# Kernel tuning notes

Measured on AMD Instinct MI355X. Metric: run time of the kernel, lower is better.

The kernel has to match this reference:

```python
import jax, jax.numpy as jnp
import numpy as np

NUM_HEADS = 8
HEAD_DIM = 64
GROUPS = 32
EPS = 1e-5


def setup_inputs() -> dict:
    key = jax.random.key(0)
    ks = jax.random.split(key, 7)
    B, C, H, W = 8, 512, 32, 32
    x = jax.random.normal(ks[0], (B, C, H, W), dtype=jnp.float32)
    gn_w = jnp.ones((C,), dtype=jnp.float32)
    gn_b = jnp.zeros((C,), dtype=jnp.float32)
    # 1x1 convs stored as [out, in] matrices
    qkv_w = jax.random.normal(ks[1], (3 * C, C), dtype=jnp.float32) * (1.0 / np.sqrt(C))
    qkv_b = jnp.zeros((3 * C,), dtype=jnp.float32)
    proj_w = jax.random.normal(ks[2], (C, C), dtype=jnp.float32) * (1.0 / np.sqrt(C))
    proj_b = jnp.zeros((C,), dtype=jnp.float32)
    return {"x": x, "gn_w": gn_w, "gn_b": gn_b, "qkv_w": qkv_w,
            "qkv_b": qkv_b, "proj_w": proj_w, "proj_b": proj_b}


def _group_norm(x, w, b):
    B, C, H, W = x.shape
    xg = x.reshape(B, GROUPS, C // GROUPS, H, W)
    mu = xg.mean(axis=(2, 3, 4), keepdims=True)
    var = xg.var(axis=(2, 3, 4), keepdims=True)
    xn = ((xg - mu) * jax.lax.rsqrt(var + EPS)).reshape(B, C, H, W)
    return xn * w[None, :, None, None] + b[None, :, None, None]


def reference(x, gn_w, gn_b, qkv_w, qkv_b, proj_w, proj_b):
    B, C, H, W = x.shape
    N = H * W
    h = _group_norm(x, gn_w, gn_b)
    # 1x1 conv == per-pixel matmul: [B, 3C, N]
    hf = h.reshape(B, C, N)
    qkv = jnp.einsum('oc,bcn->bon', qkv_w, hf) + qkv_b[None, :, None]
    qkv = qkv.reshape(B, 3, NUM_HEADS, HEAD_DIM, N)
    q, k, v = qkv[:, 0], qkv[:, 1], qkv[:, 2]  # each [B, h, d, N]
    attn = jnp.einsum('bhdi,bhdj->bhij', q, k) * (HEAD_DIM ** -0.5)
    attn = jax.nn.softmax(attn, axis=-1)
    out = jnp.einsum('bhij,bhdj->bhdi', attn, v)  # [B, h, d, N]
    out = out.reshape(B, C, N)
    out = jnp.einsum('oc,bcn->bon', proj_w, out) + proj_b[None, :, None]
    return x + out.reshape(B, C, H, W)
```

## Files before the change

### kernel.cpp

```cpp
#include <hip/hip_runtime.h>
#include <hip/hip_bf16.h>

#define BF16 __hip_bfloat16

typedef __attribute__((ext_vector_type(8))) short bf16x8;
typedef __attribute__((ext_vector_type(4))) float f32x4;
typedef __attribute__((ext_vector_type(4))) unsigned short ushort4v;
typedef __attribute__((ext_vector_type(4))) float float4v;

__device__ __forceinline__ unsigned short f2bf(float f) {
  BF16 h = __float2bfloat16(f);
  union { BF16 h; unsigned short u; } cv;
  cv.h = h;
  return cv.u;
}

__device__ __forceinline__ void gload_lds16(const BF16* g, BF16* s) {
  __builtin_amdgcn_global_load_lds(
      (const __attribute__((address_space(1))) void*)g,
      (__attribute__((address_space(3))) void*)s, 16, 0, 0);
}

__global__ __launch_bounds__(256) void cast_w_kernel(const float* __restrict__ qw,
                                                     const float* __restrict__ pw,
                                                     BF16* __restrict__ wq,
                                                     BF16* __restrict__ wp) {
  int i = blockIdx.x * 256 + threadIdx.x;
  if (i < 1536 * 512) wq[i] = __float2bfloat16(qw[i]);
  if (i < 512 * 512)  wp[i] = __float2bfloat16(pw[i]);
}

__global__ __launch_bounds__(256) void gn_kernel(const float* __restrict__ x,
                                                 const float* __restrict__ gw,
                                                 const float* __restrict__ gb,
                                                 BF16* __restrict__ h_t) {
  const int blk = blockIdx.x;
  const int bb = blk >> 5, g = blk & 31;
  const float* xg = x + (size_t)(bb * 512 + g * 16) * 1024;

  float s = 0.f, ss = 0.f;
  const float4v* x4 = (const float4v*)xg;
  for (int i = threadIdx.x; i < 4096; i += 256) {
    float4v v = x4[i];
    s  += v[0] + v[1] + v[2] + v[3];
    ss += v[0] * v[0] + v[1] * v[1] + v[2] * v[2] + v[3] * v[3];
  }
  for (int off = 32; off > 0; off >>= 1) {
    s  += __shfl_down(s, off, 64);
    ss += __shfl_down(ss, off, 64);
  }
  __shared__ float sred[8];
  const int wv = threadIdx.x >> 6;
  if ((threadIdx.x & 63) == 0) { sred[wv] = s; sred[4 + wv] = ss; }
  __syncthreads();
  const float S  = sred[0] + sred[1] + sred[2] + sred[3];
  const float SS = sred[4] + sred[5] + sred[6] + sred[7];
  const float mean = S * (1.f / 16384.f);
  const float var  = SS * (1.f / 16384.f) - mean * mean;
  const float rstd = rsqrtf(var + 1e-5f);

  const int ci = threadIdx.x & 15, nb = threadIdx.x >> 4;
  const int c  = g * 16 + ci;
  const float aw = gw[c] * rstd;
  const float ab = gb[c] - mean * aw;
  const float* xrow = xg + (size_t)ci * 1024;
  BF16* hb = h_t + (size_t)bb * 1024 * 512 + c;
  #pragma unroll 4
  for (int i = 0; i < 64; ++i) {
    int n = nb + i * 16;
    hb[(size_t)n * 512] = __float2bfloat16(aw * xrow[n] + ab);
  }
}

#define GEMM_PROLOGUE()                                                        \
  const int tid = threadIdx.x, l = tid & 63, wv = tid >> 6;                    \
  const int wm = wv >> 1, wn = wv & 1;                                         \
  const int lc = l & 15, lh = l >> 4;                                          \
  __shared__ __align__(16) BF16 Al[128 * 64];                                  \
  __shared__ __align__(16) BF16 Bl[128 * 64];                                  \
  f32x4 acc[4][4] = {};                                                        \
  int srow[4], scg[4];                                                         \
  _Pragma("unroll")                                                            \
  for (int t = 0; t < 4; ++t) {                                                \
    int cidx = t * 256 + wv * 64 + l;            \
    srow[t] = cidx >> 3;                                                       \
    scg[t]  = (cidx & 7) ^ (srow[t] & 7);    \
  }                                                                            \
  for (int kt = 0; kt < 8; ++kt) {                                             \
    const int k0 = kt * 64;                                                    \
    __syncthreads();                                                           \
    _Pragma("unroll")                                                          \
    for (int t = 0; t < 4; ++t) {                                              \
      gload_lds16(&A[(size_t)srow[t] * 512 + k0 + scg[t] * 8],                 \
                  &Al[(t * 256 + wv * 64) * 8]);                               \
      gload_lds16(&B[(size_t)srow[t] * 512 + k0 + scg[t] * 8],                 \
                  &Bl[(t * 256 + wv * 64) * 8]);                               \
    }                                                                          \
    __syncthreads();                                                           \
    _Pragma("unroll")                                                          \
    for (int ks = 0; ks < 2; ++ks) {                                           \
      bf16x8 af[4], bfr[4];                                                    \
      _Pragma("unroll")                                                        \
      for (int i = 0; i < 4; ++i) {                                            \
        int rA = wm * 64 + i * 16 + lc;                                        \
        int cA = (ks * 4 + lh) ^ (rA & 7);                                     \
        af[i] = *(const bf16x8*)&Al[(rA * 8 + cA) * 8];                        \
        int rB = wn * 64 + i * 16 + lc;                                        \
        int cB = (ks * 4 + lh) ^ (rB & 7);                                     \
        bfr[i] = *(const bf16x8*)&Bl[(rB * 8 + cB) * 8];                       \
      }                                                                        \
      _Pragma("unroll")                                                        \
      for (int i = 0; i < 4; ++i)                                              \
        _Pragma("unroll")                                                      \
        for (int j = 0; j < 4; ++j)                                            \
          acc[i][j] = __builtin_amdgcn_mfma_f32_16x16x32_bf16(af[i], bfr[j],   \
                                                              acc[i][j], 0, 0, 0); \
    }                                                                          \
  }

__global__ __launch_bounds__(256) void qkv_gemm_kernel(const BF16* __restrict__ Wq,
                                                       const BF16* __restrict__ Ht,
                                                       const float* __restrict__ bias,
                                                       BF16* __restrict__ q_t,
                                                       BF16* __restrict__ k_t,
                                                       BF16* __restrict__ v_nat) {
  const int nt = blockIdx.x, mt = blockIdx.y, b = blockIdx.z;
  const int m0 = mt * 128, n0 = nt * 128;
  const BF16* A = Wq + (size_t)m0 * 512;
  const BF16* B = Ht + (size_t)b * 1024 * 512 + (size_t)n0 * 512;
  GEMM_PROLOGUE()

  const int r0 = lh * 4;
  #pragma unroll
  for (int mi = 0; mi < 4; ++mi) {
    const int o = m0 + wm * 64 + mi * 16 + r0;
    #pragma unroll
    for (int ni = 0; ni < 4; ++ni) {
      const int pix = n0 + wn * 64 + ni * 16 + lc;
      f32x4 a = acc[mi][ni];
      if (mt < 8) {
        const float scale = (mt < 4) ? 0.125f : 1.0f;
        const int hh = (o >> 6) & 7;
        const int d = o & 63;
        BF16* dst = (mt < 4 ? q_t : k_t) +
                    ((size_t)(b * 8 + hh) * 1024 + pix) * 64 + d;
        ushort4v pk;
        #pragma unroll
        for (int r = 0; r < 4; ++r) pk[r] = f2bf((a[r] + bias[o + r]) * scale);
        *(ushort4v*)dst = pk;
      } else {
        #pragma unroll
        for (int r = 0; r < 4; ++r) {
          const int vr = o + r - 1024;
          v_nat[((size_t)(b * 512 + vr)) * 1024 + pix] =
              __float2bfloat16(a[r] + bias[o + r]);
        }
      }
    }
  }
}

__global__ __launch_bounds__(256) void proj_gemm_kernel(const BF16* __restrict__ Wp,
                                                        const BF16* __restrict__ At,
                                                        const float* __restrict__ bias,
                                                        const float* __restrict__ x,
                                                        float* __restrict__ out) {
  const int nt = blockIdx.x, mt = blockIdx.y, b = blockIdx.z;
  const int m0 = mt * 128, n0 = nt * 128;
  const BF16* A = Wp + (size_t)m0 * 512;
  const BF16* B = At + (size_t)b * 1024 * 512 + (size_t)n0 * 512;
  GEMM_PROLOGUE()

  const int r0 = lh * 4;
  #pragma unroll
  for (int mi = 0; mi < 4; ++mi) {
    #pragma unroll
    for (int ni = 0; ni < 4; ++ni) {
      const int n = n0 + wn * 64 + ni * 16 + lc;
      f32x4 a = acc[mi][ni];
      #pragma unroll
      for (int r = 0; r < 4; ++r) {
        const int c = m0 + wm * 64 + mi * 16 + r0 + r;
        const size_t idx = ((size_t)(b * 512 + c)) * 1024 + n;
        out[idx] = x[idx] + bias[c] + a[r];
      }
    }
  }
}

__global__ __launch_bounds__(256) void attn_kernel(const BF16* __restrict__ q_t,
                                                   const BF16* __restrict__ k_t,
                                                   const BF16* __restrict__ v_nat,
                                                   BF16* __restrict__ attout) {
  const int bh = blockIdx.y;
  const int b = bh >> 3, hh = bh & 7;
  const int i0 = blockIdx.x * 64;
  const int tid = threadIdx.x, l = tid & 63, wv = tid >> 6;
  const int lc = l & 15, lh = l >> 4;

  __shared__ __align__(16) BF16 Kl[2][64 * 64];
  __shared__ __align__(16) BF16 Vl[2][64 * 64];
  __shared__ __align__(16) BF16 Pl[4][16][72];

  bf16x8 aq0, aq1;
  {
    const BF16* qp = q_t + ((size_t)bh * 1024 + i0 + wv * 16 + lc) * 64;
    aq0 = *(const bf16x8*)&qp[lh * 8];
    aq1 = *(const bf16x8*)&qp[32 + lh * 8];
  }

  f32x4 O[4] = {};
  float mr = -1e30f, lr = 0.f;

  const BF16* kbase = k_t + (size_t)bh * 1024 * 64;
  const BF16* vbase = v_nat + (size_t)bh * 64 * 1024;

  int srow[2], scg[2];
  #pragma unroll
  for (int it = 0; it < 2; ++it) {
    int cidx = it * 256 + wv * 64 + l;
    srow[it] = cidx >> 3;
    scg[it]  = (cidx & 7) ^ (srow[it] & 7);
  }

  #pragma unroll
  for (int it = 0; it < 2; ++it) {
    gload_lds16(&kbase[(size_t)srow[it] * 64 + scg[it] * 8],
                &Kl[0][(it * 256 + wv * 64) * 8]);
    gload_lds16(&vbase[(size_t)srow[it] * 1024 + scg[it] * 8],
                &Vl[0][(it * 256 + wv * 64) * 8]);
  }

  for (int jt = 0; jt < 16; ++jt) {
    const int cur = jt & 1;
    __syncthreads();
    if (jt < 15) {
      const int j1 = (jt + 1) * 64, nxt = cur ^ 1;
      #pragma unroll
      for (int it = 0; it < 2; ++it) {
        gload_lds16(&kbase[(size_t)(j1 + srow[it]) * 64 + scg[it] * 8],
                    &Kl[nxt][(it * 256 + wv * 64) * 8]);
        gload_lds16(&vbase[(size_t)srow[it] * 1024 + j1 + scg[it] * 8],
                    &Vl[nxt][(it * 256 + wv * 64) * 8]);
      }
    }

    f32x4 Sv[4];
    __builtin_amdgcn_s_setprio(1);
    #pragma unroll
    for (int jf = 0; jf < 4; ++jf) {
      const int jl = jf * 16 + lc;
      int c0 = lh ^ (jl & 7);
      bf16x8 ak = *(const bf16x8*)&Kl[cur][(jl * 8 + c0) * 8];
      f32x4 s0 = {};
      s0 = __builtin_amdgcn_mfma_f32_16x16x32_bf16(ak, aq0, s0, 0, 0, 0);
      int c1 = (4 + lh) ^ (jl & 7);
      ak = *(const bf16x8*)&Kl[cur][(jl * 8 + c1) * 8];
      Sv[jf] = __builtin_amdgcn_mfma_f32_16x16x32_bf16(ak, aq1, s0, 0, 0, 0);
    }
    __builtin_amdgcn_s_setprio(0);

    float tmax = Sv[0][0];
    #pragma unroll
    for (int jf = 0; jf < 4; ++jf)
      #pragma unroll
      for (int r = 0; r < 4; ++r) tmax = fmaxf(tmax, Sv[jf][r]);
    tmax = fmaxf(tmax, __shfl_xor(tmax, 16, 64));
    tmax = fmaxf(tmax, __shfl_xor(tmax, 32, 64));
    const float mnew = fmaxf(mr, tmax);
    const float sc = __expf(mr - mnew);
    mr = mnew;
    float rs = 0.f;
    float p[4][4];
    #pragma unroll
    for (int jf = 0; jf < 4; ++jf)
      #pragma unroll
      for (int r = 0; r < 4; ++r) {
        p[jf][r] = __expf(Sv[jf][r] - mnew);
        rs += p[jf][r];
      }
    rs += __shfl_xor(rs, 16, 64);
    rs += __shfl_xor(rs, 32, 64);
    lr = lr * sc + rs;
    #pragma unroll
    for (int nf = 0; nf < 4; ++nf)
      #pragma unroll
      for (int r = 0; r < 4; ++r) O[nf][r] *= sc;

    #pragma unroll
    for (int jf = 0; jf < 4; ++jf) {
      ushort4v pk;
      #pragma unroll
      for (int r = 0; r < 4; ++r) pk[r] = f2bf(p[jf][r]);
      *(ushort4v*)&Pl[wv][lc][jf * 16 + 4 * lh] = pk;
    }
    const bf16x8 bp0 = *(const bf16x8*)&Pl[wv][lc][lh * 8];
    const bf16x8 bp1 = *(const bf16x8*)&Pl[wv][lc][32 + lh * 8];

    __builtin_amdgcn_s_setprio(1);
    #pragma unroll
    for (int nf = 0; nf < 4; ++nf) {
      const int dl = nf * 16 + lc;
      int c0 = lh ^ (dl & 7);
      bf16x8 av = *(const bf16x8*)&Vl[cur][(dl * 8 + c0) * 8];
      O[nf] = __builtin_amdgcn_mfma_f32_16x16x32_bf16(av, bp0, O[nf], 0, 0, 0);
      int c1 = (4 + lh) ^ (dl & 7);
      av = *(const bf16x8*)&Vl[cur][(dl * 8 + c1) * 8];
      O[nf] = __builtin_amdgcn_mfma_f32_16x16x32_bf16(av, bp1, O[nf], 0, 0, 0);
    }
    __builtin_amdgcn_s_setprio(0);
  }

  const float inv = 1.0f / lr;
  BF16* dst = attout + ((size_t)b * 1024 + i0 + wv * 16 + lc) * 512 + hh * 64;
  #pragma unroll
  for (int nf = 0; nf < 4; ++nf) {
    ushort4v pk;
    #pragma unroll
    for (int r = 0; r < 4; ++r) pk[r] = f2bf(O[nf][r] * inv);
    *(ushort4v*)&dst[nf * 16 + 4 * lh] = pk;
  }
}

extern "C" void kernel_launch(void* const* d_in, const int* in_sizes, int n_in,
                              void* d_out, int out_size, void* d_ws, size_t ws_size,
                              hipStream_t stream) {
  const float* x      = (const float*)d_in[0];
  const float* gn_w   = (const float*)d_in[1];
  const float* gn_b   = (const float*)d_in[2];
  const float* qkv_w  = (const float*)d_in[3];
  const float* qkv_b  = (const float*)d_in[4];
  const float* proj_w = (const float*)d_in[5];
  const float* proj_b = (const float*)d_in[6];
  float* out = (float*)d_out;

  char* ws = (char*)d_ws;
  BF16* wq    = (BF16*)(ws);
  BF16* wp    = (BF16*)(ws + 1572864);
  BF16* h_t   = (BF16*)(ws + 2097152);
  BF16* q_t   = (BF16*)(ws + 10485760);
  BF16* k_t   = (BF16*)(ws + 18874368);
  BF16* v_nat = (BF16*)(ws + 27262976);
  BF16* attout = h_t;

  cast_w_kernel<<<3072, 256, 0, stream>>>(qkv_w, proj_w, wq, wp);
  gn_kernel<<<256, 256, 0, stream>>>(x, gn_w, gn_b, h_t);
  qkv_gemm_kernel<<<dim3(8, 12, 8), 256, 0, stream>>>(wq, h_t, qkv_b, q_t, k_t, v_nat);
  attn_kernel<<<dim3(16, 64), 256, 0, stream>>>(q_t, k_t, v_nat, attout);
  proj_gemm_kernel<<<dim3(8, 4, 8), 256, 0, stream>>>(wp, attout, proj_b, x, out);
}
```

Baseline: 184.2 us.

## Remap grids for XCD locality and process two query blocks per attention wave

All kernels now use a 1D grid whose low three bits select the batch, so each XCD (blocks are dealt round-robin across the eight XCDs) works on a single batch and can reuse that batch's data in its L2. The attention kernel has each wave handle 32 query rows (two 16-row blocks), so every K/V fragment read from LDS feeds twice as many MFMAs, and the grid shrinks to 512 blocks. It also adds lazy softmax rescaling that updates the running max only when the tile max exceeds it by more than 8. That lowers rescale work but lets unnormalised exponentials grow up to e^8, and the extra live registers may reduce occupancy.

```diff
diff --git a/kernel.cpp b/kernel.cpp
--- a/kernel.cpp
+++ b/kernel.cpp
@@ -34,8 +34,8 @@
                                                  const float* __restrict__ gw,
                                                  const float* __restrict__ gb,
                                                  BF16* __restrict__ h_t) {
-  const int blk = blockIdx.x;
-  const int bb = blk >> 5, g = blk & 31;
+  const int L = blockIdx.x;
+  const int bb = L & 7, g = L >> 3;
   const float* xg = x + (size_t)(bb * 512 + g * 16) * 1024;
 
   float s = 0.f, ss = 0.f;
@@ -82,9 +82,9 @@
   int srow[4], scg[4];                                                         \
   _Pragma("unroll")                                                            \
   for (int t = 0; t < 4; ++t) {                                                \
-    int cidx = t * 256 + wv * 64 + l;            \
+    int cidx = t * 256 + wv * 64 + l;                                          \
     srow[t] = cidx >> 3;                                                       \
-    scg[t]  = (cidx & 7) ^ (srow[t] & 7);    \
+    scg[t]  = (cidx & 7) ^ (srow[t] & 7);                                      \
   }                                                                            \
   for (int kt = 0; kt < 8; ++kt) {                                             \
     const int k0 = kt * 64;                                                    \
@@ -124,7 +124,9 @@
                                                        BF16* __restrict__ q_t,
                                                        BF16* __restrict__ k_t,
                                                        BF16* __restrict__ v_nat) {
-  const int nt = blockIdx.x, mt = blockIdx.y, b = blockIdx.z;
+  const int L = blockIdx.x;
+  const int b = L & 7, w = L >> 3;
+  const int mt = w % 12, nt = w / 12;
   const int m0 = mt * 128, n0 = nt * 128;
   const BF16* A = Wq + (size_t)m0 * 512;
   const BF16* B = Ht + (size_t)b * 1024 * 512 + (size_t)n0 * 512;
@@ -165,7 +167,9 @@
                                                         const float* __restrict__ bias,
                                                         const float* __restrict__ x,
                                                         float* __restrict__ out) {
-  const int nt = blockIdx.x, mt = blockIdx.y, b = blockIdx.z;
+  const int L = blockIdx.x;
+  const int b = L & 7, w = L >> 3;
+  const int mt = w & 3, nt = w >> 2;
   const int m0 = mt * 128, n0 = nt * 128;
   const BF16* A = Wp + (size_t)m0 * 512;
   const BF16* B = At + (size_t)b * 1024 * 512 + (size_t)n0 * 512;
@@ -192,25 +196,28 @@
                                                    const BF16* __restrict__ k_t,
                                                    const BF16* __restrict__ v_nat,
                                                    BF16* __restrict__ attout) {
-  const int bh = blockIdx.y;
-  const int b = bh >> 3, hh = bh & 7;
-  const int i0 = blockIdx.x * 64;
+  const int L = blockIdx.x;
+  const int xcd = L & 7, w = L >> 3;
+  const int b = xcd, hh = w & 7;
+  const int bh = b * 8 + hh;
+  const int i0 = (w >> 3) * 128;
   const int tid = threadIdx.x, l = tid & 63, wv = tid >> 6;
   const int lc = l & 15, lh = l >> 4;
 
   __shared__ __align__(16) BF16 Kl[2][64 * 64];
   __shared__ __align__(16) BF16 Vl[2][64 * 64];
-  __shared__ __align__(16) BF16 Pl[4][16][72];
-
-  bf16x8 aq0, aq1;
-  {
-    const BF16* qp = q_t + ((size_t)bh * 1024 + i0 + wv * 16 + lc) * 64;
-    aq0 = *(const bf16x8*)&qp[lh * 8];
-    aq1 = *(const bf16x8*)&qp[32 + lh * 8];
-  }
-
-  f32x4 O[4] = {};
-  float mr = -1e30f, lr = 0.f;
+  __shared__ __align__(16) BF16 Pl[4][2][16][72];
+
+  bf16x8 aq[2][2];
+  #pragma unroll
+  for (int cb = 0; cb < 2; ++cb) {
+    const BF16* qp = q_t + ((size_t)bh * 1024 + i0 + wv * 32 + cb * 16 + lc) * 64;
+    aq[cb][0] = *(const bf16x8*)&qp[lh * 8];
+    aq[cb][1] = *(const bf16x8*)&qp[32 + lh * 8];
+  }
+
+  f32x4 O[2][4] = {};
+  float mr[2] = {-1e30f, -1e30f}, lr[2] = {0.f, 0.f};
 
   const BF16* kbase = k_t + (size_t)bh * 1024 * 64;
   const BF16* vbase = v_nat + (size_t)bh * 64 * 1024;
@@ -245,80 +252,93 @@
       }
     }
 
-    f32x4 Sv[4];
+    f32x4 Sv[2][4];
     __builtin_amdgcn_s_setprio(1);
     #pragma unroll
     for (int jf = 0; jf < 4; ++jf) {
       const int jl = jf * 16 + lc;
-      int c0 = lh ^ (jl & 7);
-      bf16x8 ak = *(const bf16x8*)&Kl[cur][(jl * 8 + c0) * 8];
-      f32x4 s0 = {};
-      s0 = __builtin_amdgcn_mfma_f32_16x16x32_bf16(ak, aq0, s0, 0, 0, 0);
-      int c1 = (4 + lh) ^ (jl & 7);
-      ak = *(const bf16x8*)&Kl[cur][(jl * 8 + c1) * 8];
-      Sv[jf] = __builtin_amdgcn_mfma_f32_16x16x32_bf16(ak, aq1, s0, 0, 0, 0);
+      const int c0 = lh ^ (jl & 7), c1 = (4 + lh) ^ (jl & 7);
+      bf16x8 ak0 = *(const bf16x8*)&Kl[cur][(jl * 8 + c0) * 8];
+      bf16x8 ak1 = *(const bf16x8*)&Kl[cur][(jl * 8 + c1) * 8];
+      #pragma unroll
+      for (int cb = 0; cb < 2; ++cb) {
+        f32x4 s0 = {};
+        s0 = __builtin_amdgcn_mfma_f32_16x16x32_bf16(ak0, aq[cb][0], s0, 0, 0, 0);
+        Sv[cb][jf] = __builtin_amdgcn_mfma_f32_16x16x32_bf16(ak1, aq[cb][1], s0, 0, 0, 0);
+      }
     }
     __builtin_amdgcn_s_setprio(0);
 
-    float tmax = Sv[0][0];
-    #pragma unroll
-    for (int jf = 0; jf < 4; ++jf)
-      #pragma unroll
-      for (int r = 0; r < 4; ++r) tmax = fmaxf(tmax, Sv[jf][r]);
-    tmax = fmaxf(tmax, __shfl_xor(tmax, 16, 64));
-    tmax = fmaxf(tmax, __shfl_xor(tmax, 32, 64));
-    const float mnew = fmaxf(mr, tmax);
-    const float sc = __expf(mr - mnew);
-    mr = mnew;
-    float rs = 0.f;
-    float p[4][4];
-    #pragma unroll
-    for (int jf = 0; jf < 4; ++jf)
-      #pragma unroll
-      for (int r = 0; r < 4; ++r) {
-        p[jf][r] = __expf(Sv[jf][r] - mnew);
-        rs += p[jf][r];
-      }
-    rs += __shfl_xor(rs, 16, 64);
-    rs += __shfl_xor(rs, 32, 64);
-    lr = lr * sc + rs;
-    #pragma unroll
-    for (int nf = 0; nf < 4; ++nf)
-      #pragma unroll
-      for (int r = 0; r < 4; ++r) O[nf][r] *= sc;
-
-    #pragma unroll
-    for (int jf = 0; jf < 4; ++jf) {
-      ushort4v pk;
-      #pragma unroll
-      for (int r = 0; r < 4; ++r) pk[r] = f2bf(p[jf][r]);
-      *(ushort4v*)&Pl[wv][lc][jf * 16 + 4 * lh] = pk;
-    }
-    const bf16x8 bp0 = *(const bf16x8*)&Pl[wv][lc][lh * 8];
-    const bf16x8 bp1 = *(const bf16x8*)&Pl[wv][lc][32 + lh * 8];
+    #pragma unroll
+    for (int cb = 0; cb < 2; ++cb) {
+      float tmax = Sv[cb][0][0];
+      #pragma unroll
+      for (int jf = 0; jf < 4; ++jf)
+        #pragma unroll
+        for (int r = 0; r < 4; ++r) tmax = fmaxf(tmax, Sv[cb][jf][r]);
+      tmax = fmaxf(tmax, __shfl_xor(tmax, 16, 64));
+      tmax = fmaxf(tmax, __shfl_xor(tmax, 32, 64));
+      if (__any(tmax > mr[cb] + 8.f)) {
+        const float mnew = fmaxf(mr[cb], tmax);
+        const float sc = __expf(mr[cb] - mnew);
+        mr[cb] = mnew;
+        lr[cb] *= sc;
+        #pragma unroll
+        for (int nf = 0; nf < 4; ++nf)
+          #pragma unroll
+          for (int r = 0; r < 4; ++r) O[cb][nf][r] *= sc;
+      }
+      float rs = 0.f;
+      #pragma unroll
+      for (int jf = 0; jf < 4; ++jf) {
+        ushort4v pk;
+        #pragma unroll
+        for (int r = 0; r < 4; ++r) {
+          float p = __expf(Sv[cb][jf][r] - mr[cb]);
+          rs += p;
+          pk[r] = f2bf(p);
+        }
+        *(ushort4v*)&Pl[wv][cb][lc][jf * 16 + 4 * lh] = pk;
+      }
+      rs += __shfl_xor(rs, 16, 64);
+      rs += __shfl_xor(rs, 32, 64);
+      lr[cb] += rs;
+    }
+
+    bf16x8 bp[2][2];
+    #pragma unroll
+    for (int cb = 0; cb < 2; ++cb) {
+      bp[cb][0] = *(const bf16x8*)&Pl[wv][cb][lc][lh * 8];
+      bp[cb][1] = *(const bf16x8*)&Pl[wv][cb][lc][32 + lh * 8];
+    }
 
     __builtin_amdgcn_s_setprio(1);
     #pragma unroll
     for (int nf = 0; nf < 4; ++nf) {
       const int dl = nf * 16 + lc;
-      int c0 = lh ^ (dl & 7);
-      bf16x8 av = *(const bf16x8*)&Vl[cur][(dl * 8 + c0) * 8];
-      O[nf] = __builtin_amdgcn_mfma_f32_16x16x32_bf16(av, bp0, O[nf], 0, 0, 0);
-      int c1 = (4 + lh) ^ (dl & 7);
-      av = *(const bf16x8*)&Vl[cur][(dl * 8 + c1) * 8];
-      O[nf] = __builtin_amdgcn_mfma_f32_16x16x32_bf16(av, bp1, O[nf], 0, 0, 0);
+      const int c0 = lh ^ (dl & 7), c1 = (4 + lh) ^ (dl & 7);
+      bf16x8 av0 = *(const bf16x8*)&Vl[cur][(dl * 8 + c0) * 8];
+      bf16x8 av1 = *(const bf16x8*)&Vl[cur][(dl * 8 + c1) * 8];
+      #pragma unroll
+      for (int cb = 0; cb < 2; ++cb) {
+        O[cb][nf] = __builtin_amdgcn_mfma_f32_16x16x32_bf16(av0, bp[cb][0], O[cb][nf], 0, 0, 0);
+        O[cb][nf] = __builtin_amdgcn_mfma_f32_16x16x32_bf16(av1, bp[cb][1], O[cb][nf], 0, 0, 0);
+      }
     }
     __builtin_amdgcn_s_setprio(0);
   }
 
-  const float inv = 1.0f / lr;
-  BF16* dst = attout + ((size_t)b * 1024 + i0 + wv * 16 + lc) * 512 + hh * 64;
-  #pragma unroll
-  for (int nf = 0; nf < 4; ++nf) {
-    ushort4v pk;
-    #pragma unroll
-    for (int r = 0; r < 4; ++r) pk[r] = f2bf(O[nf][r] * inv);
-    *(ushort4v*)&dst[nf * 16 + 4 * lh] = pk;
+  #pragma unroll
+  for (int cb = 0; cb < 2; ++cb) {
+    const float inv = 1.0f / lr[cb];
+    BF16* dst = attout + ((size_t)b * 1024 + i0 + wv * 32 + cb * 16 + lc) * 512 + hh * 64;
+    #pragma unroll
+    for (int nf = 0; nf < 4; ++nf) {
+      ushort4v pk;
+      #pragma unroll
+      for (int r = 0; r < 4; ++r) pk[r] = f2bf(O[cb][nf][r] * inv);
+      *(ushort4v*)&dst[nf * 16 + 4 * lh] = pk;
+    }
   }
 }
 
@@ -345,7 +365,7 @@
 
   cast_w_kernel<<<3072, 256, 0, stream>>>(qkv_w, proj_w, wq, wp);
   gn_kernel<<<256, 256, 0, stream>>>(x, gn_w, gn_b, h_t);
-  qkv_gemm_kernel<<<dim3(8, 12, 8), 256, 0, stream>>>(wq, h_t, qkv_b, q_t, k_t, v_nat);
-  attn_kernel<<<dim3(16, 64), 256, 0, stream>>>(q_t, k_t, v_nat, attout);
-  proj_gemm_kernel<<<dim3(8, 4, 8), 256, 0, stream>>>(wp, attout, proj_b, x, out);
-}
+  qkv_gemm_kernel<<<768, 256, 0, stream>>>(wq, h_t, qkv_b, q_t, k_t, v_nat);
+  attn_kernel<<<512, 256, 0, stream>>>(q_t, k_t, v_nat, attout);
+  proj_gemm_kernel<<<256, 256, 0, stream>>>(wp, attout, proj_b, x, out);
+}
```

Measured after the change: 174.8 us. -5.1%, faster.
